# Optimization experiments

Hardware: AMD Instinct MI355X
Metric: run time of the kernel (lower is better)

## Reference

```python
import jax, jax.numpy as jnp
import numpy as np

B, T, H, UNITS = 64, 512, 1024, 1024

def setup_inputs() -> dict:
    key = jax.random.key(0)
    ks = jax.random.split(key, 8)
    s = 0.02
    return {
        "dec_hidden": jax.random.normal(ks[0], (B, H), jnp.float32),
        "enc_output": jax.random.normal(ks[1], (B, T, H), jnp.float32),
        "Wh": jax.random.normal(ks[2], (H, UNITS), jnp.float32) * s,
        "bh": jnp.zeros((UNITS,), jnp.float32),
        "Ws": jax.random.normal(ks[3], (H, UNITS), jnp.float32) * s,
        "bs": jnp.zeros((UNITS,), jnp.float32),
        "Wv": jax.random.normal(ks[4], (UNITS, 1), jnp.float32) * s,
        "bv": jnp.zeros((1,), jnp.float32),
    }

def reference(dec_hidden, enc_output, Wh, bh, Ws, bs, Wv, bv):
    # Faithful to original: tanh applied only to W_h(enc_output) term.
    enc_proj = jnp.tanh(jnp.einsum('bth,hu->btu', enc_output, Wh) + bh)  # [B,T,U]
    dec_proj = (dec_hidden @ Ws + bs)[:, None, :]                        # [B,1,U]
    score = jnp.einsum('btu,uo->bto', enc_proj + dec_proj, Wv) + bv      # [B,T,1]
    attn_dist = jax.nn.softmax(score, axis=1)                            # [B,T,1]
    context_vector = jnp.sum(attn_dist * enc_output, axis=1)             # [B,H]
    return context_vector, jnp.squeeze(attn_dist, axis=-1)
```

## Files before the change

kernel.cpp:

```cpp
#include <hip/hip_runtime.h>
#include <hip/hip_bf16.h>

typedef unsigned short u16;
typedef __attribute__((ext_vector_type(8))) short short8;
typedef __attribute__((ext_vector_type(4))) float f32x4;

#define B_  64
#define T_  512
#define H_  1024
#define U_  1024
#define BT_ (B_*T_)

#define BM 128
#define BN 128
#define BK 32

#define GLL16(gp, lp) __builtin_amdgcn_global_load_lds( \
    (const __attribute__((address_space(1))) void*)(gp), \
    (__attribute__((address_space(3))) void*)(lp), 16, 0, 0)

template<int N>
__device__ __forceinline__ void vwait() {
  asm volatile("s_waitcnt vmcnt(%0)" :: "n"(N) : "memory");
}

__device__ __forceinline__ u16 f32_to_bf16(float f) {
  union { float f; unsigned u; } v; v.f = f;
  unsigned r = v.u + 0x7FFFu + ((v.u >> 16) & 1u);
  return (u16)(r >> 16);
}
__device__ __forceinline__ unsigned pack_bf16x2(float lo, float hi) {
  return (unsigned)f32_to_bf16(lo) | ((unsigned)f32_to_bf16(hi) << 16);
}

__global__ __launch_bounds__(256) void ba_prep(const float4* __restrict__ in,
                                               uint4* __restrict__ out,
                                               const float* __restrict__ wh,
                                               u16* __restrict__ whT,
                                               float* __restrict__ score) {
  __shared__ float tile[32][33];
  const int bx = blockIdx.x;
  const int tid = threadIdx.x;
  if (bx < 16384) {
    int i = bx * 256 + tid;
    float4 v0 = in[2 * i], v1 = in[2 * i + 1];
    uint4 o;
    o.x = pack_bf16x2(v0.x, v0.y);
    o.y = pack_bf16x2(v0.z, v0.w);
    o.z = pack_bf16x2(v1.x, v1.y);
    o.w = pack_bf16x2(v1.z, v1.w);
    out[i] = o;
    if (bx < 128) score[bx * 256 + tid] = 0.f;
  } else {
    int wb = bx - 16384;
    int u0 = (wb & 31) * 32, h0 = (wb >> 5) * 32;
    int tx = tid & 31, ty = tid >> 5;
    #pragma unroll
    for (int i = 0; i < 32; i += 8)
      tile[ty + i][tx] = wh[(long)(h0 + ty + i) * U_ + u0 + tx];
    __syncthreads();
    #pragma unroll
    for (int i = 0; i < 32; i += 8)
      whT[(long)(u0 + ty + i) * H_ + h0 + tx] = f32_to_bf16(tile[tx][ty + i]);
  }
}

__global__ __launch_bounds__(256, 3) void ba_score(
    const u16* __restrict__ A, const u16* __restrict__ Bt,
    const float* __restrict__ bh, const float* __restrict__ wv,
    float* __restrict__ score) {
  __shared__ u16 lA[3][BM * BK];
  __shared__ u16 lB[3][BN * BK];

  const int tid  = threadIdx.x;
  const int wid  = tid >> 6;
  const int lane = tid & 63;
  const int wm = wid >> 1, wn = wid & 1;
  const long row0  = (long)blockIdx.x * BM;
  const int  ncol0 = blockIdx.y * BN;

  const int c0 = 2 * wid, c1 = 2 * wid + 1;
  const int lsub = lane >> 2;
  const int csw = (((lane & 3) - ((lane >> 3) & 3)) & 3) * 8;

  const int fr = lane & 15;
  const int pofs = ((((lane >> 4) + ((lane >> 1) & 3)) & 3)) * 8;

  const u16* gA0 = A + (row0 + 16 * c0 + lsub) * H_ + csw;
  const u16* gA1 = A + (row0 + 16 * c1 + lsub) * H_ + csw;
  const u16* gB0 = Bt + (long)(ncol0 + 16 * c0 + lsub) * H_ + csw;
  const u16* gB1 = Bt + (long)(ncol0 + 16 * c1 + lsub) * H_ + csw;

  f32x4 acc[4][4];
  #pragma unroll
  for (int i = 0; i < 4; ++i)
    #pragma unroll
    for (int j = 0; j < 4; ++j) acc[i][j] = (f32x4){0.f, 0.f, 0.f, 0.f};

#define STAGE(t, b) do { \
    const int _k = (t) * BK; \
    GLL16(gA0 + _k, (char*)lA[b] + c0 * 1024); \
    GLL16(gA1 + _k, (char*)lA[b] + c1 * 1024); \
    GLL16(gB0 + _k, (char*)lB[b] + c0 * 1024); \
    GLL16(gB1 + _k, (char*)lB[b] + c1 * 1024); \
  } while (0)

#define KSTEP(s, bi, WAITN) do { \
    vwait<WAITN>(); \
    __builtin_amdgcn_sched_barrier(0); \
    __builtin_amdgcn_s_barrier(); \
    __builtin_amdgcn_sched_barrier(0); \
    short8 av[4], bvv[4]; \
    _Pragma("unroll") \
    for (int i = 0; i < 4; ++i) { \
      av[i]  = *(const short8*)&lA[bi][(wm * 64 + i * 16 + fr) * BK + pofs]; \
      bvv[i] = *(const short8*)&lB[bi][(wn * 64 + i * 16 + fr) * BK + pofs]; \
    } \
    _Pragma("unroll") \
    for (int i = 0; i < 4; ++i) \
      _Pragma("unroll") \
      for (int j = 0; j < 4; ++j) \
        acc[i][j] = __builtin_amdgcn_mfma_f32_16x16x32_bf16(av[i], bvv[j], acc[i][j], 0, 0, 0); \
    __builtin_amdgcn_sched_barrier(0); \
    __builtin_amdgcn_s_barrier(); \
    __builtin_amdgcn_sched_barrier(0); \
    if ((s) + 3 < 32) STAGE((s) + 3, bi); \
  } while (0)

  STAGE(0, 0);
  STAGE(1, 1);
  STAGE(2, 2);

  int bi = 0;
  for (int s = 0; s < 30; ++s) {
    KSTEP(s, bi, 8);
    bi = (bi == 2) ? 0 : bi + 1;
  }
  KSTEP(30, bi, 4);
  bi = (bi == 2) ? 0 : bi + 1;
  KSTEP(31, bi, 0);
#undef KSTEP
#undef STAGE

  float sloc[4][4];
  #pragma unroll
  for (int i = 0; i < 4; ++i)
    #pragma unroll
    for (int r = 0; r < 4; ++r) sloc[i][r] = 0.f;

  #pragma unroll
  for (int j = 0; j < 4; ++j) {
    const int n = ncol0 + wn * 64 + j * 16 + fr;
    const float bhn = bh[n];
    const float wvn = wv[n];
    #pragma unroll
    for (int i = 0; i < 4; ++i) {
      #pragma unroll
      for (int r = 0; r < 4; ++r) {
        float x = acc[i][j][r] + bhn;
        float e = __expf(2.f * x);
        float t = 1.f - 2.f / (e + 1.f);
        sloc[i][r] += t * wvn;
      }
    }
  }

  #pragma unroll
  for (int i = 0; i < 4; ++i) {
    #pragma unroll
    for (int r = 0; r < 4; ++r) {
      float v = sloc[i][r];
      v += __shfl_xor(v, 1);
      v += __shfl_xor(v, 2);
      v += __shfl_xor(v, 4);
      v += __shfl_xor(v, 8);
      if ((lane & 15) == 0) {
        int m = wm * 64 + i * 16 + (lane >> 4) * 4 + r;
        atomicAdd(&score[row0 + m], v);
      }
    }
  }
}

__global__ __launch_bounds__(256) void ba_context1(const float4* __restrict__ enc4,
                                                   const float* __restrict__ score,
                                                   float* __restrict__ attn_out,
                                                   float4* __restrict__ part) {
  __shared__ float redm[4], reds[4];
  __shared__ float atile[32];
  int b = blockIdx.x, c = blockIdx.y, tid = threadIdx.x;
  int lane = tid & 63, wid = tid >> 6;
  const float* s = score + b * T_;
  float v0 = s[tid], v1 = s[tid + 256];
  float m = fmaxf(v0, v1);
  #pragma unroll
  for (int o = 1; o < 64; o <<= 1) m = fmaxf(m, __shfl_xor(m, o));
  if (lane == 0) redm[wid] = m;
  __syncthreads();
  m = fmaxf(fmaxf(redm[0], redm[1]), fmaxf(redm[2], redm[3]));
  float e0 = __expf(v0 - m), e1 = __expf(v1 - m);
  float sum = e0 + e1;
  #pragma unroll
  for (int o = 1; o < 64; o <<= 1) sum += __shfl_xor(sum, o);
  if (lane == 0) reds[wid] = sum;
  __syncthreads();
  float inv = 1.f / (reds[0] + reds[1] + reds[2] + reds[3]);

  if (c == 0) {
    attn_out[b * T_ + tid] = e0 * inv;
    attn_out[b * T_ + tid + 256] = e1 * inv;
  }
  int base = c * 32;
  if (base < 256) {
    if (tid >= base && tid < base + 32) atile[tid - base] = e0 * inv;
  } else {
    int bb = base - 256;
    if (tid >= bb && tid < bb + 32) atile[tid - bb] = e1 * inv;
  }
  __syncthreads();

  const float4* e = enc4 + ((long)b * T_ + base) * (H_ / 4) + tid;
  float4 acc = {0.f, 0.f, 0.f, 0.f};
  #pragma unroll 4
  for (int t = 0; t < 32; ++t) {
    float4 v = e[(long)t * (H_ / 4)];
    float at = atile[t];
    acc.x = fmaf(at, v.x, acc.x);
    acc.y = fmaf(at, v.y, acc.y);
    acc.z = fmaf(at, v.z, acc.z);
    acc.w = fmaf(at, v.w, acc.w);
  }
  part[((long)b * 16 + c) * (H_ / 4) + tid] = acc;
}

__global__ __launch_bounds__(256) void ba_context2(const float4* __restrict__ part,
                                                   float4* __restrict__ ctx) {
  int b = blockIdx.x;
  int tid = threadIdx.x;
  const float4* p = part + (long)b * 16 * (H_ / 4) + tid;
  float4 acc = {0.f, 0.f, 0.f, 0.f};
  #pragma unroll
  for (int c = 0; c < 16; ++c) {
    float4 v = p[c * (H_ / 4)];
    acc.x += v.x; acc.y += v.y; acc.z += v.z; acc.w += v.w;
  }
  ctx[b * (H_ / 4) + tid] = acc;
}

extern "C" void kernel_launch(void* const* d_in, const int* in_sizes, int n_in,
                              void* d_out, int out_size, void* d_ws, size_t ws_size,
                              hipStream_t stream) {
  const float* enc = (const float*)d_in[1];
  const float* Wh  = (const float*)d_in[2];
  const float* bh  = (const float*)d_in[3];
  const float* Wv  = (const float*)d_in[6];

  float* out      = (float*)d_out;
  float* ctx_out  = out;
  float* attn_out = out + B_ * H_;

  char* ws = (char*)d_ws;
  u16*   encb  = (u16*)ws;
  u16*   whT   = (u16*)(ws + (size_t)67108864);
  float* score = (float*)(ws + (size_t)67108864 + 2097152);
  float* part  = (float*)(ws + (size_t)67108864 + 2097152 + 131072);

  ba_prep<<<16384 + 1024, 256, 0, stream>>>((const float4*)enc, (uint4*)encb,
                                            Wh, whT, score);
  ba_score<<<dim3(BT_ / BM, U_ / BN), 256, 0, stream>>>(encb, whT, bh, Wv, score);
  ba_context1<<<dim3(B_, 16), 256, 0, stream>>>((const float4*)enc, score,
                                                attn_out, (float4*)part);
  ba_context2<<<B_, 256, 0, stream>>>((const float4*)part, (float4*)ctx_out);
}
```

Measured before the change: 323.1 us.

## Enlarge score GEMM tile to 256x256 with 512 threads and interleaved loads

```diff
diff --git a/kernel.cpp b/kernel.cpp
--- a/kernel.cpp
+++ b/kernel.cpp
@@ -11,8 +11,8 @@
 #define U_  1024
 #define BT_ (B_*T_)
 
-#define BM 128
-#define BN 128
+#define BM 256
+#define BN 256
 #define BK 32
 
 #define GLL16(gp, lp) __builtin_amdgcn_global_load_lds( \
@@ -65,118 +65,136 @@
   }
 }
 
-__global__ __launch_bounds__(256, 3) void ba_score(
+__global__ __launch_bounds__(512, 2) void ba_score(
     const u16* __restrict__ A, const u16* __restrict__ Bt,
     const float* __restrict__ bh, const float* __restrict__ wv,
     float* __restrict__ score) {
-  __shared__ u16 lA[3][BM * BK];
-  __shared__ u16 lB[3][BN * BK];
+  __shared__ u16 lA[4][BM * BK];
+  __shared__ u16 lB[4][BN * BK];
 
   const int tid  = threadIdx.x;
   const int wid  = tid >> 6;
   const int lane = tid & 63;
-  const int wm = wid >> 1, wn = wid & 1;
+  const int wm = wid >> 2;
+  const int wn = wid & 3;
   const long row0  = (long)blockIdx.x * BM;
   const int  ncol0 = blockIdx.y * BN;
 
-  const int c0 = 2 * wid, c1 = 2 * wid + 1;
-  const int lsub = lane >> 2;
-  const int csw = (((lane & 3) - ((lane >> 3) & 3)) & 3) * 8;
+  const int srow = tid >> 2;
+  const int csw  = (((tid & 3) - ((tid >> 3) & 3)) & 3) * 8;
 
   const int fr = lane & 15;
-  const int pofs = ((((lane >> 4) + ((lane >> 1) & 3)) & 3)) * 8;
-
-  const u16* gA0 = A + (row0 + 16 * c0 + lsub) * H_ + csw;
-  const u16* gA1 = A + (row0 + 16 * c1 + lsub) * H_ + csw;
-  const u16* gB0 = Bt + (long)(ncol0 + 16 * c0 + lsub) * H_ + csw;
-  const u16* gB1 = Bt + (long)(ncol0 + 16 * c1 + lsub) * H_ + csw;
-
-  f32x4 acc[4][4];
-  #pragma unroll
-  for (int i = 0; i < 4; ++i)
+  const int pofs = (((lane >> 4) + ((lane >> 1) & 3)) & 3) * 8;
+  const int aBase = (wm * 128 + fr) * BK + pofs;
+  const int bBase = (wn * 64  + fr) * BK + pofs;
+
+  const u16* gA = A  + (row0 + srow) * H_ + csw;
+  const u16* gB = Bt + (long)(ncol0 + srow) * H_ + csw;
+
+  f32x4 acc[8][4];
+  #pragma unroll
+  for (int i = 0; i < 8; ++i)
     #pragma unroll
     for (int j = 0; j < 4; ++j) acc[i][j] = (f32x4){0.f, 0.f, 0.f, 0.f};
 
-#define STAGE(t, b) do { \
-    const int _k = (t) * BK; \
-    GLL16(gA0 + _k, (char*)lA[b] + c0 * 1024); \
-    GLL16(gA1 + _k, (char*)lA[b] + c1 * 1024); \
-    GLL16(gB0 + _k, (char*)lB[b] + c0 * 1024); \
-    GLL16(gB1 + _k, (char*)lB[b] + c1 * 1024); \
+#define STAGEF(t_, b_) do { \
+    const long _k = (long)(t_) * BK; \
+    GLL16(gA + _k,            (char*)lA[b_] + wid * 1024); \
+    GLL16(gA + 128 * H_ + _k, (char*)lA[b_] + 8192 + wid * 1024); \
+    GLL16(gB + _k,            (char*)lB[b_] + wid * 1024); \
+    GLL16(gB + 128 * H_ + _k, (char*)lB[b_] + 8192 + wid * 1024); \
   } while (0)
 
-#define KSTEP(s, bi, WAITN) do { \
+#define TILE(t_, WAITN, DO_STAGE) do { \
+    const int _bt = (t_) & 3; \
     vwait<WAITN>(); \
     __builtin_amdgcn_sched_barrier(0); \
     __builtin_amdgcn_s_barrier(); \
     __builtin_amdgcn_sched_barrier(0); \
-    short8 av[4], bvv[4]; \
-    _Pragma("unroll") \
-    for (int i = 0; i < 4; ++i) { \
-      av[i]  = *(const short8*)&lA[bi][(wm * 64 + i * 16 + fr) * BK + pofs]; \
-      bvv[i] = *(const short8*)&lB[bi][(wn * 64 + i * 16 + fr) * BK + pofs]; \
+    short8 bfrag[4], afrag[4]; \
+    _Pragma("unroll") \
+    for (int nf = 0; nf < 4; ++nf) \
+      bfrag[nf] = *(const short8*)&lB[_bt][bBase + nf * 512]; \
+    _Pragma("unroll") \
+    for (int mf = 0; mf < 4; ++mf) \
+      afrag[mf] = *(const short8*)&lA[_bt][aBase + mf * 512]; \
+    if (DO_STAGE) { \
+      const long _k = (long)((t_) + 3) * BK; \
+      const int _nb = ((t_) + 3) & 3; \
+      GLL16(gA + _k,            (char*)lA[_nb] + wid * 1024); \
+      GLL16(gA + 128 * H_ + _k, (char*)lA[_nb] + 8192 + wid * 1024); \
     } \
-    _Pragma("unroll") \
-    for (int i = 0; i < 4; ++i) \
+    __builtin_amdgcn_s_setprio(1); \
+    _Pragma("unroll") \
+    for (int mf = 0; mf < 4; ++mf) \
       _Pragma("unroll") \
-      for (int j = 0; j < 4; ++j) \
-        acc[i][j] = __builtin_amdgcn_mfma_f32_16x16x32_bf16(av[i], bvv[j], acc[i][j], 0, 0, 0); \
-    __builtin_amdgcn_sched_barrier(0); \
-    __builtin_amdgcn_s_barrier(); \
-    __builtin_amdgcn_sched_barrier(0); \
-    if ((s) + 3 < 32) STAGE((s) + 3, bi); \
+      for (int nf = 0; nf < 4; ++nf) \
+        acc[mf][nf] = __builtin_amdgcn_mfma_f32_16x16x32_bf16(afrag[mf], bfrag[nf], acc[mf][nf], 0, 0, 0); \
+    __builtin_amdgcn_s_setprio(0); \
+    _Pragma("unroll") \
+    for (int mf = 0; mf < 4; ++mf) \
+      afrag[mf] = *(const short8*)&lA[_bt][aBase + (4 + mf) * 512]; \
+    if (DO_STAGE) { \
+      const long _k = (long)((t_) + 3) * BK; \
+      const int _nb = ((t_) + 3) & 3; \
+      GLL16(gB + _k,            (char*)lB[_nb] + wid * 1024); \
+      GLL16(gB + 128 * H_ + _k, (char*)lB[_nb] + 8192 + wid * 1024); \
+    } \
+    __builtin_amdgcn_s_setprio(1); \
+    _Pragma("unroll") \
+    for (int mf = 0; mf < 4; ++mf) \
+      _Pragma("unroll") \
+      for (int nf = 0; nf < 4; ++nf) \
+        acc[4 + mf][nf] = __builtin_amdgcn_mfma_f32_16x16x32_bf16(afrag[mf], bfrag[nf], acc[4 + mf][nf], 0, 0, 0); \
+    __builtin_amdgcn_s_setprio(0); \
   } while (0)
 
-  STAGE(0, 0);
-  STAGE(1, 1);
-  STAGE(2, 2);
-
-  int bi = 0;
-  for (int s = 0; s < 30; ++s) {
-    KSTEP(s, bi, 8);
-    bi = (bi == 2) ? 0 : bi + 1;
-  }
-  KSTEP(30, bi, 4);
-  bi = (bi == 2) ? 0 : bi + 1;
-  KSTEP(31, bi, 0);
-#undef KSTEP
-#undef STAGE
-
-  float sloc[4][4];
-  #pragma unroll
-  for (int i = 0; i < 4; ++i)
-    #pragma unroll
-    for (int r = 0; r < 4; ++r) sloc[i][r] = 0.f;
-
-  #pragma unroll
-  for (int j = 0; j < 4; ++j) {
-    const int n = ncol0 + wn * 64 + j * 16 + fr;
+  STAGEF(0, 0);
+  STAGEF(1, 1);
+  STAGEF(2, 2);
+
+  for (int t = 0; t < 30; ++t) {
+    TILE(t, 8, t < 29);
+  }
+  TILE(30, 4, false);
+  TILE(31, 0, false);
+#undef TILE
+#undef STAGEF
+
+  float sloc[8][4];
+  #pragma unroll
+  for (int mf = 0; mf < 8; ++mf)
+    #pragma unroll
+    for (int r = 0; r < 4; ++r) sloc[mf][r] = 0.f;
+
+  #pragma unroll
+  for (int nf = 0; nf < 4; ++nf) {
+    const int n = ncol0 + wn * 64 + nf * 16 + fr;
     const float bhn = bh[n];
     const float wvn = wv[n];
     #pragma unroll
-    for (int i = 0; i < 4; ++i) {
+    for (int mf = 0; mf < 8; ++mf) {
       #pragma unroll
       for (int r = 0; r < 4; ++r) {
-        float x = acc[i][j][r] + bhn;
+        float x = acc[mf][nf][r] + bhn;
         float e = __expf(2.f * x);
-        float t = 1.f - 2.f / (e + 1.f);
-        sloc[i][r] += t * wvn;
+        sloc[mf][r] += (1.f - 2.f / (e + 1.f)) * wvn;
       }
     }
   }
 
   #pragma unroll
-  for (int i = 0; i < 4; ++i) {
+  for (int mf = 0; mf < 8; ++mf) {
     #pragma unroll
     for (int r = 0; r < 4; ++r) {
-      float v = sloc[i][r];
+      float v = sloc[mf][r];
       v += __shfl_xor(v, 1);
       v += __shfl_xor(v, 2);
       v += __shfl_xor(v, 4);
       v += __shfl_xor(v, 8);
       if ((lane & 15) == 0) {
-        int m = wm * 64 + i * 16 + (lane >> 4) * 4 + r;
-        atomicAdd(&score[row0 + m], v);
+        long m = row0 + wm * 128 + mf * 16 + (lane >> 4) * 4 + r;
+        atomicAdd(&score[m], v);
       }
     }
   }
@@ -267,7 +285,7 @@
 
   ba_prep<<<16384 + 1024, 256, 0, stream>>>((const float4*)enc, (uint4*)encb,
                                             Wh, whT, score);
-  ba_score<<<dim3(BT_ / BM, U_ / BN), 256, 0, stream>>>(encb, whT, bh, Wv, score);
+  ba_score<<<dim3(BT_ / BM, U_ / BN), 512, 0, stream>>>(encb, whT, bh, Wv, score);
   ba_context1<<<dim3(B_, 16), 256, 0, stream>>>((const float4*)enc, score,
                                                 attn_out, (float4*)part);
   ba_context2<<<B_, 256, 0, stream>>>((const float4*)part, (float4*)ctx_out);
```

Measured after the change: 323.0 us. Within noise of the previous version (-0.0%).
